# Optimization experiments

Hardware: AMD Instinct MI355X
Metric: run time of the kernel (lower is better)

The kernel has to match this reference:

```python
import math
import jax, jax.numpy as jnp
import numpy as np

B, N, T, H, DIN, NH = 4, 256, 30, 128, 3, 8
BN = B * N
DH = H // NH


def _pos_embed(t, h):
    pos = np.arange(t)[:, None].astype(np.float64)
    div = np.exp(np.arange(0, h, 2) * (-math.log(10000.0) / h))
    pe = np.zeros((t, h), np.float32)
    pe[:, 0::2] = np.sin(pos * div)
    pe[:, 1::2] = np.cos(pos * div)
    return jnp.asarray(pe)


def setup_inputs() -> dict:
    key = jax.random.key(0)
    ks = jax.random.split(key, 24)
    lin = lambda k, i, o: (jax.random.normal(k, (i, o), jnp.float32) / np.sqrt(i).astype(np.float32))
    vec = lambda k, o: jax.random.normal(k, (o,), jnp.float32) * 0.02
    return dict(
        x_raw=jax.random.normal(ks[0], (T, BN, DIN), jnp.float32),
        adjacency=jax.random.bernoulli(ks[1], 0.01, (T, BN, BN)).astype(jnp.float32),
        ego_mask=jax.random.bernoulli(ks[2], 0.5, (B, T, N)),
        W1=lin(ks[3], DIN, H), b1=vec(ks[4], H),
        W2=lin(ks[5], H, H), b2=vec(ks[6], H),
        Wq=lin(ks[7], H, H), bq=vec(ks[8], H),
        Wk=lin(ks[9], H, H), bk=vec(ks[10], H),
        Wv=lin(ks[11], H, H), bv=vec(ks[12], H),
        Wqi=lin(ks[13], H, H), bqi=vec(ks[14], H),
        Wki=lin(ks[15], H, H), bki=vec(ks[16], H),
        Wvi=lin(ks[17], H, H), bvi=vec(ks[18], H),
        Wo=lin(ks[19], H, H), bo=vec(ks[20], H),
    )


def reference(x_raw, adjacency, ego_mask,
              W1, b1, W2, b2,
              Wq, bq, Wk, bk, Wv, bv,
              Wqi, bqi, Wki, bki, Wvi, bvi,
              Wo, bo):
    # (B,T,N) -> (T, B*N) node-active mask, matching permute(1,0,2).reshape
    mask_flat = ego_mask.transpose(1, 0, 2).reshape(T, BN).astype(x_raw.dtype)

    def step(_, inp):
        x_t, A_t, m = inp  # (BN,DIN), (BN,BN), (BN,)
        # mask rows/cols (equiv. to gather A[idx][:,idx]) and add self loops
        A = A_t * m[:, None] * m[None, :] + jnp.diag(m)
        deg = A.sum(axis=1)
        dinv = jnp.where(deg > 0, 1.0, 0.0) * jax.lax.rsqrt(jnp.where(deg > 0, deg, 1.0))
        An = dinv[:, None] * A * dinv[None, :]  # D^-1/2 (A+I) D^-1/2
        h1 = jax.nn.relu(An @ (x_t @ W1) + b1)
        h2 = jax.nn.relu(An @ (h1 @ W2) + b2) * m[:, None]  # scatter back into zeros
        return None, h2

    _, hs = jax.lax.scan(step, None, (x_raw, adjacency, mask_flat))  # (T,BN,H)

    x_seq = hs.transpose(1, 0, 2) + _pos_embed(T, H)  # (BN,T,H)
    Q = x_seq @ Wq + bq
    K = x_seq @ Wk + bk
    V = x_seq @ Wv + bv
    # nn.MultiheadAttention applies its own in-projection to Q/K/V
    q = (Q @ Wqi + bqi).reshape(BN, T, NH, DH)
    k = (K @ Wki + bki).reshape(BN, T, NH, DH)
    v = (V @ Wvi + bvi).reshape(BN, T, NH, DH)
    attn = jax.nn.softmax(jnp.einsum('bthd,bshd->bhts', q, k) / np.sqrt(DH).astype(np.float32), axis=-1)
    o = jnp.einsum('bhts,bshd->bthd', attn, v).reshape(BN, T, H)
    out = (o @ Wo + bo).reshape(B, N, T, H)
    return out
```

## Files before the change

### kernel.cpp

```cpp
#include <hip/hip_runtime.h>
#include <hip/hip_bf16.h>
#include <math.h>

#define TT  30
#define BNN 1024
#define HH  128
#define MT  (TT*BNN)
#define CAP 64

typedef short bf16x8 __attribute__((ext_vector_type(8)));
typedef float f32x4 __attribute__((ext_vector_type(4)));

#if defined(__has_builtin)
#if __has_builtin(__builtin_amdgcn_global_load_lds)
#define HAS_GLL 1
#endif
#endif

#ifdef HAS_GLL
typedef const __attribute__((address_space(1))) unsigned int* gas1_t;
typedef __attribute__((address_space(3))) unsigned int* las3_t;
__device__ __forceinline__ void gload16(const void* g, void* l) {
  __builtin_amdgcn_global_load_lds((gas1_t)g, (las3_t)l, 16, 0, 0);
}
#endif

__device__ __forceinline__ float ldf(const void* p, size_t i, int fp) {
  if (fp == 0) {
    unsigned int w = ((unsigned int)(((const unsigned short*)p)[i])) << 16;
    float f; __builtin_memcpy(&f, &w, 4); return f;
  }
  return ((const float*)p)[i];
}
__device__ __forceinline__ float bf2f(unsigned short u) {
  unsigned int w = ((unsigned int)u) << 16;
  float f; __builtin_memcpy(&f, &w, 4); return f;
}
__device__ __forceinline__ unsigned short f2bf(float f) {
  unsigned int u; __builtin_memcpy(&u, &f, 4);
  return (unsigned short)((u + 0x7FFFu + ((u >> 16) & 1u)) >> 16);
}
__device__ __forceinline__ void splitbf(float a, unsigned short& h, unsigned short& l) {
  h = f2bf(a);
  l = f2bf(a - bf2f(h));
}

__device__ int block_detect_fp(const unsigned short* xw) {
  __shared__ int cnt_exp;
  if (threadIdx.x == 0) cnt_exp = 0;
  __syncthreads();
  int local = 0;
  for (int i = threadIdx.x; i < 2048; i += 256) {
    int e = (xw[i] >> 8) & 0x7F;
    if (e >= 0x3A && e <= 0x41) local++;
  }
  atomicAdd(&cnt_exp, local);
  __syncthreads();
  return (cnt_exp > 1536) ? 0 : 1;
}
__device__ int block_detect_ego(const unsigned int* ew) {
  __shared__ int f_odd1, f_any, f_nz;
  if (threadIdx.x == 0) { f_odd1 = 0; f_any = 0; f_nz = 0; }
  __syncthreads();
  int l1 = 0, l2 = 0, l3 = 0;
  for (int i = threadIdx.x; i < 7680; i += 256) {
    unsigned int w = ew[i];
    #pragma unroll
    for (int e = 0; e < 4; ++e) {
      unsigned char b = (w >> (8 * e)) & 0xff;
      if (b == 0x3F) { l2 = 1; if (e == 1) l1 = 1; }
      if (b != 0 && e != 0) l3 = 1;
    }
  }
  if (l1) atomicOr(&f_odd1, 1);
  if (l2) atomicOr(&f_any, 1);
  if (l3) atomicOr(&f_nz, 1);
  __syncthreads();
  return f_odd1 ? 0 : (f_any ? 1 : (f_nz ? 2 : 3));
}

__global__ __launch_bounds__(256) void setup_kernel(
    const void* x_raw, const void* ego,
    const void* W1, const void* b1, const void* W2, const void* b2, const void* Wo, const void* bo,
    const void* Wq, const void* bq, const void* Wk, const void* bk, const void* Wv, const void* bv,
    const void* Wqi, const void* bqi, const void* Wki, const void* bki, const void* Wvi, const void* bvi,
    int* mode, float* pe, float* W1f, float* b1f, float* b2f, float* bof,
    unsigned short* W2h, unsigned short* W2l, unsigned short* Woh, unsigned short* Wol,
    unsigned short* Wch, unsigned short* Wcl, float* bqkv, float* maskf) {
  int bid = blockIdx.x;
  if (bid == 0) {
    int fp = block_detect_fp((const unsigned short*)x_raw);
    int mm = block_detect_ego((const unsigned int*)ego);
    if (threadIdx.x == 0) { mode[0] = fp; mode[1] = mm; }
    return;
  }
  if (bid < 16) {
    int idx = (bid - 1) * 256 + threadIdx.x;
    int t = idx >> 7, i = idx & 127, j = i >> 1;
    double div = exp((double)(2 * j) * (-log(10000.0) / 128.0));
    double ang = (double)t * div;
    pe[idx] = (i & 1) ? (float)cos(ang) : (float)sin(ang);
    return;
  }
  if (bid < 147) {
    int fp = block_detect_fp((const unsigned short*)x_raw);
    int idx = (bid - 16) * 256 + threadIdx.x;
    if (idx < 16384) { int k = idx >> 7, h = idx & 127; splitbf(ldf(W2, idx, fp), W2h[h * 128 + k], W2l[h * 128 + k]); return; }
    idx -= 16384;
    if (idx < 16384) { int k = idx >> 7, h = idx & 127; splitbf(ldf(Wo, idx, fp), Woh[h * 128 + k], Wol[h * 128 + k]); return; }
    idx -= 16384;
    if (idx < 384) { W1f[idx] = ldf(W1, idx, fp); return; } idx -= 384;
    if (idx < 128) { b1f[idx] = ldf(b1, idx, fp); return; } idx -= 128;
    if (idx < 128) { b2f[idx] = ldf(b2, idx, fp); return; } idx -= 128;
    if (idx < 128) { bof[idx] = ldf(bo, idx, fp); return; }
    return;
  }
  if (bid < 267) {
    int mm = block_detect_ego((const unsigned int*)ego);
    int idx = (bid - 147) * 256 + threadIdx.x;
    int t = idx >> 10, p = idx & 1023, b = p >> 8, n = p & 255;
    size_t e = (size_t)b * (TT * 256) + (size_t)t * 256 + n;
    bool nz;
    if      (mm == 0) nz = ((const unsigned short*)ego)[e] != 0;
    else if (mm == 1) nz = ((const float*)ego)[e] != 0.f;
    else if (mm == 2) nz = ((const unsigned char*)ego)[e] != 0;
    else              nz = ((const int*)ego)[e] != 0;
    maskf[idx] = nz ? 1.f : 0.f;
    return;
  }
  int fp = block_detect_fp((const unsigned short*)x_raw);
  int cb = bid - 267;
  int g = cb / 65;
  const void* Wa = (g == 0) ? Wq : (g == 1) ? Wk : Wv;
  const void* ba = (g == 0) ? bq : (g == 1) ? bk : bv;
  const void* Wb = (g == 0) ? Wqi : (g == 1) ? Wki : Wvi;
  const void* bb = (g == 0) ? bqi : (g == 1) ? bki : bvi;
  unsigned short* Wh = Wch + (size_t)g * 16384;
  unsigned short* Wl = Wcl + (size_t)g * 16384;
  float* bc = bqkv + g * 128;
  int idx = (cb % 65) * 256 + threadIdx.x;
  if (idx < 16384) {
    int k = idx >> 7, h = idx & 127;
    float s = 0.f;
    #pragma unroll 8
    for (int m = 0; m < 128; ++m) s += ldf(Wa, k * 128 + m, fp) * ldf(Wb, m * 128 + h, fp);
    splitbf(s, Wh[h * 128 + k], Wl[h * 128 + k]);
  } else if (idx < 16512) {
    int h = idx - 16384;
    float s = ldf(bb, h, fp);
    #pragma unroll 8
    for (int m = 0; m < 128; ++m) s += ldf(ba, m, fp) * ldf(Wb, m * 128 + h, fp);
    bc[h] = s;
  }
}

__global__ __launch_bounds__(256) void csr_kernel(const void* A, const int* mode, const float* maskf,
                                                  int* nnz, int* cols, float* dinv) {
  int fp = mode[0];
  int r = blockIdx.x * 4 + (threadIdx.x >> 6);
  int lane = threadIdx.x & 63;
  int t = r >> 10, i = r & 1023;
  int tb = t << 10;
  if (maskf[r] == 0.f) { if (lane == 0) { nnz[r] = 0; dinv[r] = 0.f; } return; }
  int* myc = cols + (size_t)r * CAP;
  int cnt = 0;
  unsigned long long lmask = (1ull << lane) - 1ull;
  if (fp == 1) {
    const float* Ar = (const float*)A + (size_t)t * BNN * BNN + (size_t)i * BNN;
    #pragma unroll
    for (int it = 0; it < 4; ++it) {
      int j0 = it * 256 + lane * 4;
      float4 av = *(const float4*)(Ar + j0);
      float4 mv = *(const float4*)(maskf + tb + j0);
      float va[4] = {av.x * mv.x, av.y * mv.y, av.z * mv.z, av.w * mv.w};
      #pragma unroll
      for (int e = 0; e < 4; ++e) {
        bool hit = va[e] != 0.f;
        unsigned long long bal = __ballot(hit);
        if (hit) { int pos = cnt + __popcll(bal & lmask); if (pos < CAP) myc[pos] = j0 + e; }
        cnt += __popcll(bal);
      }
    }
  } else {
    const unsigned short* Ar = (const unsigned short*)A + (size_t)t * BNN * BNN + (size_t)i * BNN;
    #pragma unroll
    for (int it = 0; it < 2; ++it) {
      int j0 = it * 512 + lane * 8;
      uint4 av = *(const uint4*)(Ar + j0);
      unsigned int wv[4] = {av.x, av.y, av.z, av.w};
      float4 m0 = *(const float4*)(maskf + tb + j0);
      float4 m1 = *(const float4*)(maskf + tb + j0 + 4);
      float mm[8] = {m0.x, m0.y, m0.z, m0.w, m1.x, m1.y, m1.z, m1.w};
      #pragma unroll
      for (int e = 0; e < 8; ++e) {
        unsigned short u = (wv[e >> 1] >> ((e & 1) * 16)) & 0xffff;
        bool hit = (u != 0) && (mm[e] != 0.f);
        unsigned long long bal = __ballot(hit);
        if (hit) { int pos = cnt + __popcll(bal & lmask); if (pos < CAP) myc[pos] = j0 + e; }
        cnt += __popcll(bal);
      }
    }
  }
  if (lane == 0) { nnz[r] = cnt > CAP ? CAP : cnt; dinv[r] = rsqrtf((float)cnt + 1.0f); }
}

__global__ __launch_bounds__(256) void spmm1_kernel(const void* x, const int* mode, const int* nnz,
    const int* cols, const float* dinv, const float* W1f, const float* b1f,
    unsigned short* h1h, unsigned short* h1l) {
  int fp = mode[0];
  int r = blockIdx.x * 4 + (threadIdx.x >> 6);
  int lane = threadIdx.x & 63;
  int tbase = (r >> 10) << 10;
  int n = nnz[r];
  float s0 = 0.f, s1 = 0.f, s2 = 0.f;
  int j = -1;
  if (lane < n) j = tbase + cols[(size_t)r * CAP + lane];
  else if (lane == n) j = r;
  if (j >= 0) {
    float dj = dinv[j];
    s0 = dj * ldf(x, (size_t)j * 3 + 0, fp);
    s1 = dj * ldf(x, (size_t)j * 3 + 1, fp);
    s2 = dj * ldf(x, (size_t)j * 3 + 2, fp);
  }
  #pragma unroll
  for (int d = 1; d < 64; d <<= 1) {
    s0 += __shfl_xor(s0, d);
    s1 += __shfl_xor(s1, d);
    s2 += __shfl_xor(s2, d);
  }
  float dr = dinv[r];
  #pragma unroll
  for (int u = 0; u < 2; ++u) {
    int h = lane + u * 64;
    float v = dr * (s0 * W1f[h] + s1 * W1f[128 + h] + s2 * W1f[256 + h]) + b1f[h];
    splitbf(fmaxf(v, 0.f), h1h[(size_t)r * 128 + h], h1l[(size_t)r * 128 + h]);
  }
}

__global__ __launch_bounds__(256) void spmm2_kernel(const float* g2s, const int* nnz, const int* cols,
    const float* dinv, const float* b2f, const float* maskf, const float* pe,
    unsigned short* xh, unsigned short* xl) {
  int r = blockIdx.x * 4 + (threadIdx.x >> 6);
  int lane = threadIdx.x & 63;
  int c = lane * 2;
  int t = r >> 10, i = r & 1023;
  int n = nnz[r];
  const int* myc = cols + (size_t)r * CAP;
  const float* st = g2s + ((size_t)(t << 10)) * 128;
  float2 acc = *(const float2*)(g2s + (size_t)r * 128 + c);
  for (int s = 0; s < n; ++s) {
    float2 v = *(const float2*)(st + (size_t)myc[s] * 128 + c);
    acc.x += v.x; acc.y += v.y;
  }
  float dr = dinv[r], m = maskf[r];
  float2 b = *(const float2*)(b2f + c);
  float2 p = *(const float2*)(pe + t * 128 + c);
  float vx = fmaxf(dr * acc.x + b.x, 0.f) * m + p.x;
  float vy = fmaxf(dr * acc.y + b.y, 0.f) * m + p.y;
  size_t o = ((size_t)i * TT + t) * 128 + c;
  splitbf(vx, xh[o], xl[o]);
  splitbf(vy, xh[o + 1], xl[o + 1]);
}

__global__ __launch_bounds__(256) void mfma_gemm(const unsigned short* Ahi, const unsigned short* Alo,
    const unsigned short* Bhi, const unsigned short* Blo,
    const float* scale, const float* bias, float* outf, void* outfin, const int* mode) {
  __shared__ __align__(16) unsigned short Ah[64 * 64];
  __shared__ __align__(16) unsigned short Al[64 * 64];
  __shared__ __align__(16) unsigned short Bh[128 * 64];
  __shared__ __align__(16) unsigned short Bl[128 * 64];
  int tid = threadIdx.x;
  int rowTile = blockIdx.x * 64;
  int gy = blockIdx.y;
  const unsigned short* Bhp = Bhi + (size_t)gy * 16384;
  const unsigned short* Blp = Blo + (size_t)gy * 16384;
  const float* bp = bias ? (bias + gy * 128) : nullptr;
  float* ofp = outf ? (outf + (size_t)gy * ((size_t)MT * 128)) : nullptr;

  int lane = tid & 63;
  int wid = tid >> 6;
  int wrow = (wid >> 1) * 32, wcol = (wid & 1) * 64;
  f32x4 acc[2][4];
  #pragma unroll
  for (int m = 0; m < 2; ++m)
    #pragma unroll
    for (int n = 0; n < 4; ++n) acc[m][n] = (f32x4){0.f, 0.f, 0.f, 0.f};

  for (int kb = 0; kb < 2; ++kb) {
    __syncthreads();
#ifdef HAS_GLL
    {
      int lrow = lane >> 3;
      int cc = (lane & 7) ^ lrow;
      int soff = kb * 128 + cc * 16;
      #pragma unroll
      for (int i = 0; i < 2; ++i) {
        int c = wid * 2 + i;
        size_t gb = (size_t)(rowTile + c * 8 + lrow) * 256 + soff;
        gload16((const char*)Ahi + gb, (char*)Ah + c * 1024);
        gload16((const char*)Alo + gb, (char*)Al + c * 1024);
      }
      #pragma unroll
      for (int i = 0; i < 4; ++i) {
        int c = wid * 4 + i;
        size_t gb = (size_t)(c * 8 + lrow) * 256 + soff;
        gload16((const char*)Bhp + gb, (char*)Bh + c * 1024);
        gload16((const char*)Blp + gb, (char*)Bl + c * 1024);
      }
    }
#else
    #pragma unroll
    for (int it = 0; it < 2; ++it) {
      int c = it * 256 + tid;
      int r = c >> 3, cc = c & 7;
      int swz = (cc ^ (r & 7)) * 16;
      size_t src = (size_t)(rowTile + r) * 128 + kb * 64 + cc * 8;
      *(uint4*)((char*)Ah + r * 128 + swz) = *(const uint4*)(Ahi + src);
      *(uint4*)((char*)Al + r * 128 + swz) = *(const uint4*)(Alo + src);
    }
    #pragma unroll
    for (int it = 0; it < 4; ++it) {
      int c = it * 256 + tid;
      int r = c >> 3, cc = c & 7;
      int swz = (cc ^ (r & 7)) * 16;
      *(uint4*)((char*)Bh + r * 128 + swz) = *(const uint4*)(Bhp + (size_t)r * 128 + kb * 64 + cc * 8);
      *(uint4*)((char*)Bl + r * 128 + swz) = *(const uint4*)(Blp + (size_t)r * 128 + kb * 64 + cc * 8);
    }
#endif
    __syncthreads();
    #pragma unroll
    for (int ks = 0; ks < 2; ++ks) {
      bf16x8 ah[2], al[2], bh[4], bl[4];
      #pragma unroll
      for (int m = 0; m < 2; ++m) {
        int R = wrow + m * 16 + (lane & 15);
        int cc = ks * 4 + (lane >> 4);
        int off = R * 128 + ((cc ^ (R & 7)) * 16);
        ah[m] = *(const bf16x8*)((const char*)Ah + off);
        al[m] = *(const bf16x8*)((const char*)Al + off);
      }
      #pragma unroll
      for (int n = 0; n < 4; ++n) {
        int R = wcol + n * 16 + (lane & 15);
        int cc = ks * 4 + (lane >> 4);
        int off = R * 128 + ((cc ^ (R & 7)) * 16);
        bh[n] = *(const bf16x8*)((const char*)Bh + off);
        bl[n] = *(const bf16x8*)((const char*)Bl + off);
      }
      #pragma unroll
      for (int m = 0; m < 2; ++m)
        #pragma unroll
        for (int n = 0; n < 4; ++n) {
          acc[m][n] = __builtin_amdgcn_mfma_f32_16x16x32_bf16(ah[m], bl[n], acc[m][n], 0, 0, 0);
          acc[m][n] = __builtin_amdgcn_mfma_f32_16x16x32_bf16(al[m], bh[n], acc[m][n], 0, 0, 0);
          acc[m][n] = __builtin_amdgcn_mfma_f32_16x16x32_bf16(ah[m], bh[n], acc[m][n], 0, 0, 0);
        }
    }
  }
  int fp = mode[0];
  #pragma unroll
  for (int m = 0; m < 2; ++m) {
    #pragma unroll
    for (int n = 0; n < 4; ++n) {
      int col = wcol + n * 16 + (lane & 15);
      float bv = bp ? bp[col] : 0.f;
      #pragma unroll
      for (int q = 0; q < 4; ++q) {
        int row = rowTile + wrow + m * 16 + (lane >> 4) * 4 + q;
        float v = acc[m][n][q];
        if (scale) v *= scale[row];
        v += bv;
        size_t o = (size_t)row * 128 + col;
        if (ofp)           ofp[o] = v;
        else if (fp == 0)  ((unsigned short*)outfin)[o] = f2bf(v);
        else               ((float*)outfin)[o] = v;
      }
    }
  }
}

__global__ __launch_bounds__(256) void attn_kernel(const float* Q, const float* K, const float* V,
                                                   unsigned short* obh, unsigned short* obl) {
  __shared__ __align__(16) float ksm[TT * 128];
  __shared__ __align__(16) float vsm[TT * 128];
  int tid = threadIdx.x;
  size_t base = (size_t)blockIdx.x * (TT * 128);
  for (int i = tid; i < TT * 128 / 4; i += 256) {
    ((float4*)ksm)[i] = ((const float4*)(K + base))[i];
    ((float4*)vsm)[i] = ((const float4*)(V + base))[i];
  }
  int h = tid >> 5, t = tid & 31;
  float q[16];
  if (t < TT) {
    const float4* qp = (const float4*)(Q + base + (size_t)t * 128 + h * 16);
    #pragma unroll
    for (int e = 0; e < 4; ++e) { float4 f = qp[e]; q[4*e] = f.x; q[4*e+1] = f.y; q[4*e+2] = f.z; q[4*e+3] = f.w; }
  }
  __syncthreads();
  if (t >= TT) return;
  float p[TT];
  float mx = -1e30f;
  #pragma unroll
  for (int s = 0; s < TT; ++s) {
    const float4* kp = (const float4*)&ksm[s * 128 + h * 16];
    float d = 0.f;
    #pragma unroll
    for (int e = 0; e < 4; ++e) {
      float4 f = kp[e];
      d += q[4*e] * f.x + q[4*e+1] * f.y + q[4*e+2] * f.z + q[4*e+3] * f.w;
    }
    p[s] = d * 0.25f;
    mx = fmaxf(mx, p[s]);
  }
  float sum = 0.f;
  #pragma unroll
  for (int s = 0; s < TT; ++s) { p[s] = __expf(p[s] - mx); sum += p[s]; }
  float inv = 1.f / sum;
  float o[16];
  #pragma unroll
  for (int e = 0; e < 16; ++e) o[e] = 0.f;
  #pragma unroll
  for (int s = 0; s < TT; ++s) {
    const float4* vp = (const float4*)&vsm[s * 128 + h * 16];
    float ps = p[s] * inv;
    #pragma unroll
    for (int e = 0; e < 4; ++e) {
      float4 f = vp[e];
      o[4*e] += ps * f.x; o[4*e+1] += ps * f.y; o[4*e+2] += ps * f.z; o[4*e+3] += ps * f.w;
    }
  }
  unsigned short hi[16], lo[16];
  #pragma unroll
  for (int e = 0; e < 16; ++e) splitbf(o[e], hi[e], lo[e]);
  size_t oo = base + (size_t)t * 128 + h * 16;
  uint4 ph0, ph1, pl0, pl1;
  ph0.x = hi[0] | ((unsigned)hi[1] << 16);  ph0.y = hi[2] | ((unsigned)hi[3] << 16);
  ph0.z = hi[4] | ((unsigned)hi[5] << 16);  ph0.w = hi[6] | ((unsigned)hi[7] << 16);
  ph1.x = hi[8] | ((unsigned)hi[9] << 16);  ph1.y = hi[10] | ((unsigned)hi[11] << 16);
  ph1.z = hi[12] | ((unsigned)hi[13] << 16); ph1.w = hi[14] | ((unsigned)hi[15] << 16);
  pl0.x = lo[0] | ((unsigned)lo[1] << 16);  pl0.y = lo[2] | ((unsigned)lo[3] << 16);
  pl0.z = lo[4] | ((unsigned)lo[5] << 16);  pl0.w = lo[6] | ((unsigned)lo[7] << 16);
  pl1.x = lo[8] | ((unsigned)lo[9] << 16);  pl1.y = lo[10] | ((unsigned)lo[11] << 16);
  pl1.z = lo[12] | ((unsigned)lo[13] << 16); pl1.w = lo[14] | ((unsigned)lo[15] << 16);
  *(uint4*)(obh + oo) = ph0; *(uint4*)(obh + oo + 8) = ph1;
  *(uint4*)(obl + oo) = pl0; *(uint4*)(obl + oo + 8) = pl1;
}

extern "C" void kernel_launch(void* const* d_in, const int* in_sizes, int n_in,
                              void* d_out, int out_size, void* d_ws, size_t ws_size,
                              hipStream_t stream) {
  (void)in_sizes; (void)n_in; (void)out_size;
  const void* x_raw = d_in[0];
  const void* adj   = d_in[1];
  const void* ego   = d_in[2];
  const void* W1 = d_in[3];  const void* b1 = d_in[4];
  const void* W2 = d_in[5];  const void* b2 = d_in[6];
  const void* Wq = d_in[7];  const void* bq = d_in[8];
  const void* Wk = d_in[9];  const void* bk = d_in[10];
  const void* Wv = d_in[11]; const void* bv = d_in[12];
  const void* Wqi = d_in[13]; const void* bqi = d_in[14];
  const void* Wki = d_in[15]; const void* bki = d_in[16];
  const void* Wvi = d_in[17]; const void* bvi = d_in[18];
  const void* Wo = d_in[19]; const void* bo = d_in[20];

  char* w = (char*)d_ws;
  auto alloc = [&](size_t b) { char* p = w; w += (b + 255) & ~(size_t)255; return p; };
  int*   mode  = (int*)  alloc(16);
  float* maskf = (float*)alloc((size_t)MT * 4);
  float* dinv  = (float*)alloc((size_t)MT * 4);
  float* pe    = (float*)alloc((size_t)TT * HH * 4);
  float* W1f   = (float*)alloc(384 * 4);
  float* b1f   = (float*)alloc(128 * 4);
  float* b2f   = (float*)alloc(128 * 4);
  float* bof   = (float*)alloc(128 * 4);
  unsigned short* W2h = (unsigned short*)alloc(16384 * 2);
  unsigned short* W2l = (unsigned short*)alloc(16384 * 2);
  unsigned short* Woh = (unsigned short*)alloc(16384 * 2);
  unsigned short* Wol = (unsigned short*)alloc(16384 * 2);
  unsigned short* Wch = (unsigned short*)alloc((size_t)3 * 16384 * 2);
  unsigned short* Wcl = (unsigned short*)alloc((size_t)3 * 16384 * 2);
  float* bqkv  = (float*)alloc(3 * 128 * 4);
  int*   nnz   = (int*)  alloc((size_t)MT * 4);
  int*   cols  = (int*)  alloc((size_t)MT * CAP * 4);
  unsigned short* h1h = (unsigned short*)alloc((size_t)MT * 128 * 2);
  unsigned short* h1l = (unsigned short*)alloc((size_t)MT * 128 * 2);
  unsigned short* xh  = (unsigned short*)alloc((size_t)MT * 128 * 2);
  unsigned short* xl  = (unsigned short*)alloc((size_t)MT * 128 * 2);
  unsigned short* obh = (unsigned short*)alloc((size_t)MT * 128 * 2);
  unsigned short* obl = (unsigned short*)alloc((size_t)MT * 128 * 2);
  float* g2s   = (float*)alloc((size_t)MT * 128 * 4);
  float* qkv   = (float*)alloc((size_t)3 * MT * 128 * 4);
  size_t need = (size_t)(w - (char*)d_ws);
  if (need > ws_size) return;

  setup_kernel<<<462, 256, 0, stream>>>(x_raw, ego, W1, b1, W2, b2, Wo, bo,
                                        Wq, bq, Wk, bk, Wv, bv, Wqi, bqi, Wki, bki, Wvi, bvi,
                                        mode, pe, W1f, b1f, b2f, bof,
                                        W2h, W2l, Woh, Wol, Wch, Wcl, bqkv, maskf);
  csr_kernel<<<MT / 4, 256, 0, stream>>>(adj, mode, maskf, nnz, cols, dinv);
  spmm1_kernel<<<MT / 4, 256, 0, stream>>>(x_raw, mode, nnz, cols, dinv, W1f, b1f, h1h, h1l);
  mfma_gemm<<<480, 256, 0, stream>>>(h1h, h1l, W2h, W2l, dinv, nullptr, g2s, nullptr, mode);
  spmm2_kernel<<<MT / 4, 256, 0, stream>>>(g2s, nnz, cols, dinv, b2f, maskf, pe, xh, xl);
  mfma_gemm<<<dim3(480, 3), 256, 0, stream>>>(xh, xl, Wch, Wcl, nullptr, bqkv, qkv, nullptr, mode);
  attn_kernel<<<BNN, 256, 0, stream>>>(qkv, qkv + (size_t)MT * 128, qkv + (size_t)2 * MT * 128, obh, obl);
  mfma_gemm<<<480, 256, 0, stream>>>(obh, obl, Woh, Wol, nullptr, bof, nullptr, d_out, mode);
}
```

Baseline: 128.1 us.

## Fuse all pipeline stages into one cooperative persistent kernel with grid syncs

Turns each stage kernel (setup, CSR build, two SpMMs, three GEMMs, attention) into a device body function. A new cooperative mega-kernel runs them in sequence, with blocks walking the original block indices and grid.sync between stages. The aim is to remove per-launch overhead and the inter-kernel gaps. The cost is that one kernel must carry the maximum register and shared-memory footprint of all stages, which lowers occupancy, and each grid-wide barrier has its own cost. The original multi-launch path stays as a fallback if the cooperative launch fails.

Measured after the change: 216.0 us. 1.69x slower.

```diff
diff --git a/kernel.cpp b/kernel.cpp
--- a/kernel.cpp
+++ b/kernel.cpp
@@ -1,6 +1,9 @@
 #include <hip/hip_runtime.h>
 #include <hip/hip_bf16.h>
+#include <hip/hip_cooperative_groups.h>
 #include <math.h>
+
+namespace cg = cooperative_groups;
 
 #define TT  30
 #define BNN 1024
@@ -79,7 +82,8 @@
   return f_odd1 ? 0 : (f_any ? 1 : (f_nz ? 2 : 3));
 }
 
-__global__ __launch_bounds__(256) void setup_kernel(
+
+__device__ void setup_body(int bid,
     const void* x_raw, const void* ego,
     const void* W1, const void* b1, const void* W2, const void* b2, const void* Wo, const void* bo,
     const void* Wq, const void* bq, const void* Wk, const void* bk, const void* Wv, const void* bv,
@@ -87,7 +91,6 @@
     int* mode, float* pe, float* W1f, float* b1f, float* b2f, float* bof,
     unsigned short* W2h, unsigned short* W2l, unsigned short* Woh, unsigned short* Wol,
     unsigned short* Wch, unsigned short* Wcl, float* bqkv, float* maskf) {
-  int bid = blockIdx.x;
   if (bid == 0) {
     int fp = block_detect_fp((const unsigned short*)x_raw);
     int mm = block_detect_ego((const unsigned int*)ego);
@@ -154,10 +157,10 @@
   }
 }
 
-__global__ __launch_bounds__(256) void csr_kernel(const void* A, const int* mode, const float* maskf,
-                                                  int* nnz, int* cols, float* dinv) {
+__device__ void csr_body(int rblk, const void* A, const int* mode, const float* maskf,
+                         int* nnz, int* cols, float* dinv) {
   int fp = mode[0];
-  int r = blockIdx.x * 4 + (threadIdx.x >> 6);
+  int r = rblk * 4 + (threadIdx.x >> 6);
   int lane = threadIdx.x & 63;
   int t = r >> 10, i = r & 1023;
   int tb = t << 10;
@@ -204,11 +207,11 @@
   if (lane == 0) { nnz[r] = cnt > CAP ? CAP : cnt; dinv[r] = rsqrtf((float)cnt + 1.0f); }
 }
 
-__global__ __launch_bounds__(256) void spmm1_kernel(const void* x, const int* mode, const int* nnz,
+__device__ void spmm1_body(int rblk, const void* x, const int* mode, const int* nnz,
     const int* cols, const float* dinv, const float* W1f, const float* b1f,
     unsigned short* h1h, unsigned short* h1l) {
   int fp = mode[0];
-  int r = blockIdx.x * 4 + (threadIdx.x >> 6);
+  int r = rblk * 4 + (threadIdx.x >> 6);
   int lane = threadIdx.x & 63;
   int tbase = (r >> 10) << 10;
   int n = nnz[r];
@@ -237,10 +240,10 @@
   }
 }
 
-__global__ __launch_bounds__(256) void spmm2_kernel(const float* g2s, const int* nnz, const int* cols,
+__device__ void spmm2_body(int rblk, const float* g2s, const int* nnz, const int* cols,
     const float* dinv, const float* b2f, const float* maskf, const float* pe,
     unsigned short* xh, unsigned short* xl) {
-  int r = blockIdx.x * 4 + (threadIdx.x >> 6);
+  int r = rblk * 4 + (threadIdx.x >> 6);
   int lane = threadIdx.x & 63;
   int c = lane * 2;
   int t = r >> 10, i = r & 1023;
@@ -262,16 +265,16 @@
   splitbf(vy, xh[o + 1], xl[o + 1]);
 }
 
-__global__ __launch_bounds__(256) void mfma_gemm(const unsigned short* Ahi, const unsigned short* Alo,
+__device__ void gemm_body(char* smem, int rowTileIdx, int gy,
+    const unsigned short* Ahi, const unsigned short* Alo,
     const unsigned short* Bhi, const unsigned short* Blo,
     const float* scale, const float* bias, float* outf, void* outfin, const int* mode) {
-  __shared__ __align__(16) unsigned short Ah[64 * 64];
-  __shared__ __align__(16) unsigned short Al[64 * 64];
-  __shared__ __align__(16) unsigned short Bh[128 * 64];
-  __shared__ __align__(16) unsigned short Bl[128 * 64];
+  unsigned short* Ah = (unsigned short*)smem;
+  unsigned short* Al = (unsigned short*)(smem + 8192);
+  unsigned short* Bh = (unsigned short*)(smem + 16384);
+  unsigned short* Bl = (unsigned short*)(smem + 32768);
   int tid = threadIdx.x;
-  int rowTile = blockIdx.x * 64;
-  int gy = blockIdx.y;
+  int rowTile = rowTileIdx * 64;
   const unsigned short* Bhp = Bhi + (size_t)gy * 16384;
   const unsigned short* Blp = Blo + (size_t)gy * 16384;
   const float* bp = bias ? (bias + gy * 128) : nullptr;
@@ -379,12 +382,13 @@
   }
 }
 
-__global__ __launch_bounds__(256) void attn_kernel(const float* Q, const float* K, const float* V,
-                                                   unsigned short* obh, unsigned short* obl) {
-  __shared__ __align__(16) float ksm[TT * 128];
-  __shared__ __align__(16) float vsm[TT * 128];
+__device__ void attn_body(char* smem, int p, const float* Q, const float* K, const float* V,
+                          unsigned short* obh, unsigned short* obl) {
+  float* ksm = (float*)smem;
+  float* vsm = (float*)(smem + 15360);
   int tid = threadIdx.x;
-  size_t base = (size_t)blockIdx.x * (TT * 128);
+  size_t base = (size_t)p * (TT * 128);
+  __syncthreads();
   for (int i = tid; i < TT * 128 / 4; i += 256) {
     ((float4*)ksm)[i] = ((const float4*)(K + base))[i];
     ((float4*)vsm)[i] = ((const float4*)(V + base))[i];
@@ -398,7 +402,7 @@
   }
   __syncthreads();
   if (t >= TT) return;
-  float p[TT];
+  float pr[TT];
   float mx = -1e30f;
   #pragma unroll
   for (int s = 0; s < TT; ++s) {
@@ -409,12 +413,12 @@
       float4 f = kp[e];
       d += q[4*e] * f.x + q[4*e+1] * f.y + q[4*e+2] * f.z + q[4*e+3] * f.w;
     }
-    p[s] = d * 0.25f;
-    mx = fmaxf(mx, p[s]);
+    pr[s] = d * 0.25f;
+    mx = fmaxf(mx, pr[s]);
   }
   float sum = 0.f;
   #pragma unroll
-  for (int s = 0; s < TT; ++s) { p[s] = __expf(p[s] - mx); sum += p[s]; }
+  for (int s = 0; s < TT; ++s) { pr[s] = __expf(pr[s] - mx); sum += pr[s]; }
   float inv = 1.f / sum;
   float o[16];
   #pragma unroll
@@ -422,7 +426,7 @@
   #pragma unroll
   for (int s = 0; s < TT; ++s) {
     const float4* vp = (const float4*)&vsm[s * 128 + h * 16];
-    float ps = p[s] * inv;
+    float ps = pr[s] * inv;
     #pragma unroll
     for (int e = 0; e < 4; ++e) {
       float4 f = vp[e];
@@ -445,6 +449,92 @@
   *(uint4*)(obh + oo) = ph0; *(uint4*)(obh + oo + 8) = ph1;
   *(uint4*)(obl + oo) = pl0; *(uint4*)(obl + oo + 8) = pl1;
 }
+
+
+__global__ __launch_bounds__(256) void setup_kernel(
+    const void* x_raw, const void* ego,
+    const void* W1, const void* b1, const void* W2, const void* b2, const void* Wo, const void* bo,
+    const void* Wq, const void* bq, const void* Wk, const void* bk, const void* Wv, const void* bv,
+    const void* Wqi, const void* bqi, const void* Wki, const void* bki, const void* Wvi, const void* bvi,
+    int* mode, float* pe, float* W1f, float* b1f, float* b2f, float* bof,
+    unsigned short* W2h, unsigned short* W2l, unsigned short* Woh, unsigned short* Wol,
+    unsigned short* Wch, unsigned short* Wcl, float* bqkv, float* maskf) {
+  setup_body(blockIdx.x, x_raw, ego, W1, b1, W2, b2, Wo, bo, Wq, bq, Wk, bk, Wv, bv,
+             Wqi, bqi, Wki, bki, Wvi, bvi, mode, pe, W1f, b1f, b2f, bof,
+             W2h, W2l, Woh, Wol, Wch, Wcl, bqkv, maskf);
+}
+__global__ __launch_bounds__(256) void csr_kernel(const void* A, const int* mode, const float* maskf,
+                                                  int* nnz, int* cols, float* dinv) {
+  csr_body(blockIdx.x, A, mode, maskf, nnz, cols, dinv);
+}
+__global__ __launch_bounds__(256) void spmm1_kernel(const void* x, const int* mode, const int* nnz,
+    const int* cols, const float* dinv, const float* W1f, const float* b1f,
+    unsigned short* h1h, unsigned short* h1l) {
+  spmm1_body(blockIdx.x, x, mode, nnz, cols, dinv, W1f, b1f, h1h, h1l);
+}
+__global__ __launch_bounds__(256) void spmm2_kernel(const float* g2s, const int* nnz, const int* cols,
+    const float* dinv, const float* b2f, const float* maskf, const float* pe,
+    unsigned short* xh, unsigned short* xl) {
+  spmm2_body(blockIdx.x, g2s, nnz, cols, dinv, b2f, maskf, pe, xh, xl);
+}
+__global__ __launch_bounds__(256) void mfma_gemm(const unsigned short* Ahi, const unsigned short* Alo,
+    const unsigned short* Bhi, const unsigned short* Blo,
+    const float* scale, const float* bias, float* outf, void* outfin, const int* mode) {
+  __shared__ __align__(16) char smem[49152];
+  gemm_body(smem, blockIdx.x, blockIdx.y, Ahi, Alo, Bhi, Blo, scale, bias, outf, outfin, mode);
+}
+__global__ __launch_bounds__(256) void attn_kernel(const float* Q, const float* K, const float* V,
+                                                   unsigned short* obh, unsigned short* obl) {
+  __shared__ __align__(16) char smem[30720];
+  attn_body(smem, blockIdx.x, Q, K, V, obh, obl);
+}
+
+
+struct MegaArgs {
+  const void *x_raw, *adj, *ego;
+  const void *W1, *b1, *W2, *b2, *Wo, *bo;
+  const void *Wq, *bq, *Wk, *bk, *Wv, *bv;
+  const void *Wqi, *bqi, *Wki, *bki, *Wvi, *bvi;
+  int* mode; float* pe; float *W1f, *b1f, *b2f, *bof;
+  unsigned short *W2h, *W2l, *Woh, *Wol, *Wch, *Wcl;
+  float *bqkv, *maskf, *dinv;
+  int *nnz, *cols;
+  unsigned short *h1h, *h1l, *xh, *xl, *obh, *obl;
+  float *g2s, *qkv;
+  void* outfin;
+};
+
+__global__ __launch_bounds__(256) void mega_kernel(MegaArgs a) {
+  cg::grid_group grid = cg::this_grid();
+  __shared__ __align__(16) char smem[49152];
+  int nb = gridDim.x;
+  for (int b = blockIdx.x; b < 462; b += nb)
+    setup_body(b, a.x_raw, a.ego, a.W1, a.b1, a.W2, a.b2, a.Wo, a.bo, a.Wq, a.bq, a.Wk, a.bk,
+               a.Wv, a.bv, a.Wqi, a.bqi, a.Wki, a.bki, a.Wvi, a.bvi, a.mode, a.pe, a.W1f, a.b1f,
+               a.b2f, a.bof, a.W2h, a.W2l, a.Woh, a.Wol, a.Wch, a.Wcl, a.bqkv, a.maskf);
+  grid.sync();
+  for (int b = blockIdx.x; b < MT / 4; b += nb)
+    csr_body(b, a.adj, a.mode, a.maskf, a.nnz, a.cols, a.dinv);
+  grid.sync();
+  for (int b = blockIdx.x; b < MT / 4; b += nb)
+    spmm1_body(b, a.x_raw, a.mode, a.nnz, a.cols, a.dinv, a.W1f, a.b1f, a.h1h, a.h1l);
+  grid.sync();
+  for (int b = blockIdx.x; b < 480; b += nb)
+    gemm_body(smem, b, 0, a.h1h, a.h1l, a.W2h, a.W2l, a.dinv, nullptr, a.g2s, nullptr, a.mode);
+  grid.sync();
+  for (int b = blockIdx.x; b < MT / 4; b += nb)
+    spmm2_body(b, a.g2s, a.nnz, a.cols, a.dinv, a.b2f, a.maskf, a.pe, a.xh, a.xl);
+  grid.sync();
+  for (int b = blockIdx.x; b < 1440; b += nb)
+    gemm_body(smem, b % 480, b / 480, a.xh, a.xl, a.Wch, a.Wcl, nullptr, a.bqkv, a.qkv, nullptr, a.mode);
+  grid.sync();
+  for (int b = blockIdx.x; b < BNN; b += nb)
+    attn_body(smem, b, a.qkv, a.qkv + (size_t)MT * 128, a.qkv + (size_t)2 * MT * 128, a.obh, a.obl);
+  grid.sync();
+  for (int b = blockIdx.x; b < 480; b += nb)
+    gemm_body(smem, b, 0, a.obh, a.obl, a.Woh, a.Wol, nullptr, a.bof, nullptr, a.outfin, a.mode);
+}
+
 
 extern "C" void kernel_launch(void* const* d_in, const int* in_sizes, int n_in,
                               void* d_out, int out_size, void* d_ws, size_t ws_size,
@@ -493,6 +583,34 @@
   size_t need = (size_t)(w - (char*)d_ws);
   if (need > ws_size) return;
 
+  int dev = 0, coopAttr = 0, numCU = 0, maxB = 0;
+  bool coop = (hipGetDevice(&dev) == hipSuccess)
+    && (hipDeviceGetAttribute(&coopAttr, hipDeviceAttributeCooperativeLaunch, dev) == hipSuccess)
+    && coopAttr
+    && (hipDeviceGetAttribute(&numCU, hipDeviceAttributeMultiprocessorCount, dev) == hipSuccess)
+    && numCU > 0
+    && (hipOccupancyMaxActiveBlocksPerMultiprocessor(&maxB, mega_kernel, 256, 0) == hipSuccess)
+    && maxB > 0;
+  if (coop) {
+    MegaArgs ma;
+    ma.x_raw = x_raw; ma.adj = adj; ma.ego = ego;
+    ma.W1 = W1; ma.b1 = b1; ma.W2 = W2; ma.b2 = b2; ma.Wo = Wo; ma.bo = bo;
+    ma.Wq = Wq; ma.bq = bq; ma.Wk = Wk; ma.bk = bk; ma.Wv = Wv; ma.bv = bv;
+    ma.Wqi = Wqi; ma.bqi = bqi; ma.Wki = Wki; ma.bki = bki; ma.Wvi = Wvi; ma.bvi = bvi;
+    ma.mode = mode; ma.pe = pe; ma.W1f = W1f; ma.b1f = b1f; ma.b2f = b2f; ma.bof = bof;
+    ma.W2h = W2h; ma.W2l = W2l; ma.Woh = Woh; ma.Wol = Wol; ma.Wch = Wch; ma.Wcl = Wcl;
+    ma.bqkv = bqkv; ma.maskf = maskf; ma.dinv = dinv;
+    ma.nnz = nnz; ma.cols = cols;
+    ma.h1h = h1h; ma.h1l = h1l; ma.xh = xh; ma.xl = xl; ma.obh = obh; ma.obl = obl;
+    ma.g2s = g2s; ma.qkv = qkv;
+    ma.outfin = d_out;
+    int grid = maxB * numCU;
+    if (grid > 2048) grid = 2048;
+    void* params[] = { &ma };
+    if (hipLaunchCooperativeKernel(mega_kernel, dim3(grid), dim3(256), params, 0, stream) == hipSuccess)
+      return;
+  }
+
   setup_kernel<<<462, 256, 0, stream>>>(x_raw, ego, W1, b1, W2, b2, Wo, bo,
                                         Wq, bq, Wk, bk, Wv, bv, Wqi, bqi, Wki, bki, Wvi, bvi,
                                         mode, pe, W1f, b1f, b2f, bof,
```
